# Kernel optimization log

Hardware: AMD Instinct MI355X
Metric: run time of the kernel (lower is better)

The kernel has to match this reference:

```python
import jax, jax.numpy as jnp
import numpy as np
import math

B, T, D = 2, 2048, 1024
H = 16
d = D // H
I = 2816
RMS_EPS = 1e-6
GN_EPS = 1e-5


def setup_inputs() -> dict:
    key = jax.random.key(0)
    ks = jax.random.split(key, 12)
    s = 0.02
    gammas = 1.0 - jnp.exp(jnp.linspace(math.log(0.1), math.log(0.001), H)).astype(jnp.float32)
    return {
        "x": jax.random.normal(ks[0], (B, T, D), dtype=jnp.float32),
        "ln1_w": jnp.ones((D,), jnp.float32),
        "ln2_w": jnp.ones((D,), jnp.float32),
        "Wq": jax.random.normal(ks[1], (D, D), jnp.float32) * s,
        "Wk": jax.random.normal(ks[2], (D, D), jnp.float32) * s,
        "Wv": jax.random.normal(ks[3], (D, D), jnp.float32) * s,
        "Wg": jax.random.normal(ks[4], (D, D), jnp.float32) * s,
        "Wo": jax.random.normal(ks[5], (D, D), jnp.float32) * s,
        "gamma": gammas,
        "gn_w": jnp.ones((D,), jnp.float32),
        "gn_b": jnp.zeros((D,), jnp.float32),
        "gate_w": jax.random.normal(ks[6], (I, D), jnp.float32) * s,
        "up_w": jax.random.normal(ks[7], (I, D), jnp.float32) * s,
        "down_w": jax.random.normal(ks[8], (D, I), jnp.float32) * s,
    }


def _rmsnorm(x, w):
    var = jnp.mean(x * x, axis=-1, keepdims=True)
    return (x * jax.lax.rsqrt(var + RMS_EPS)) * w


def _retnet_scan(q, k, v, gamma):
    # q,k,v: (B,T,H,d); gamma: (H,)
    qT = jnp.moveaxis(q, 1, 0)  # (T,B,H,d)
    kT = jnp.moveaxis(k, 1, 0)
    vT = jnp.moveaxis(v, 1, 0)

    def step(S, qkv_t):
        q_t, k_t, v_t = qkv_t
        # S: (B,H,d,d) ; outer product k_t v_t^T
        S = gamma[None, :, None, None] * S + k_t[..., :, None] * v_t[..., None, :]
        o_t = jnp.einsum('bhd,bhde->bhe', q_t, S)
        return S, o_t

    S0 = jnp.zeros((q.shape[0], H, d, d), q.dtype)
    _, yT = jax.lax.scan(step, S0, (qT, kT, vT))  # yT: (T,B,H,d)
    return jnp.moveaxis(yT, 0, 1)  # (B,T,H,d)


def _group_norm(y, gn_w, gn_b):
    # y: (B,T,H,d). torch GroupNorm(H groups) on (B,D,T): normalize per (b, head)
    # over the (T, d) extent.
    mean = jnp.mean(y, axis=(1, 3), keepdims=True)
    var = jnp.var(y, axis=(1, 3), keepdims=True)
    yn = (y - mean) * jax.lax.rsqrt(var + GN_EPS)
    return yn * gn_w.reshape(1, 1, H, d) + gn_b.reshape(1, 1, H, d)


def reference(x, ln1_w, ln2_w, Wq, Wk, Wv, Wg, Wo, gamma, gn_w, gn_b, gate_w, up_w, down_w):
    Bx, Tx, Dx = x.shape
    h = _rmsnorm(x, ln1_w)
    q = (h @ Wq.T).reshape(Bx, Tx, H, d)
    k = (h @ Wk.T).reshape(Bx, Tx, H, d)
    v = (h @ Wv.T).reshape(Bx, Tx, H, d)
    g = jax.nn.sigmoid(h @ Wg.T)
    gam = jax.nn.sigmoid(gamma)
    y = _retnet_scan(q, k, v, gam)          # (B,T,H,d)
    y = _group_norm(y, gn_w, gn_b).reshape(Bx, Tx, Dx)
    y = g * y
    x = x + y @ Wo.T
    h2 = _rmsnorm(x, ln2_w)
    mlp = (jax.nn.silu(h2 @ gate_w.T) * (h2 @ up_w.T)) @ down_w.T
    return x + mlp
```

## Files before the change

### kernel.cpp

```cpp
#include <hip/hip_runtime.h>
#include <hip/hip_bf16.h>
#include <cstdint>
#include <cstddef>

typedef __bf16 bf16_t;
typedef __bf16 bf16x4 __attribute__((ext_vector_type(4)));
typedef __bf16 bf16x8 __attribute__((ext_vector_type(8)));
typedef float f32x4 __attribute__((ext_vector_type(4)));

#define DEVINL __device__ __forceinline__

#define TT 2048
#define DD 1024
#define HH 16
#define II 2816

DEVINL float waveSum(float v) {
#pragma unroll
  for (int m = 32; m >= 1; m >>= 1) v += __shfl_xor(v, m, 64);
  return v;
}

DEVINL float sigmoidf_(float z) { return 1.0f / (1.0f + __expf(-z)); }

DEVINL void gload_lds16(const bf16_t* g, bf16_t* l) {
  __builtin_amdgcn_global_load_lds((const __attribute__((address_space(1))) void*)g,
                                   (__attribute__((address_space(3))) void*)l, 16, 0, 0);
}

__global__ __launch_bounds__(256) void prep_kernel(const float* __restrict__ Wq,
                                                   const float* __restrict__ Wk,
                                                   const float* __restrict__ Wv,
                                                   const float* __restrict__ Wg,
                                                   const float* __restrict__ Wo,
                                                   const float* __restrict__ gate_w,
                                                   const float* __restrict__ up_w,
                                                   const float* __restrict__ down_w,
                                                   bf16_t* __restrict__ Wqkvg_bf,
                                                   bf16_t* __restrict__ Wo_bf,
                                                   bf16_t* __restrict__ GU_bf,
                                                   bf16_t* __restrict__ down_bf,
                                                   float* __restrict__ stats) {
  const int bid = blockIdx.x;
  const int tid = threadIdx.x;
  if (bid == 0 && tid < 64) stats[tid] = 0.f;
  if (bid < 5120) {
    const int which = bid >> 10;
    const float* src;
    bf16_t* dst;
    switch (which) {
      case 0: src = Wq; dst = Wqkvg_bf; break;
      case 1: src = Wk; dst = Wqkvg_bf + (size_t)DD * DD; break;
      case 2: src = Wv; dst = Wqkvg_bf + 2 * (size_t)DD * DD; break;
      case 3: src = Wg; dst = Wqkvg_bf + 3 * (size_t)DD * DD; break;
      default: src = Wo; dst = Wo_bf; break;
    }
    const int i = (bid & 1023) * 256 + tid;
    float4 v = reinterpret_cast<const float4*>(src)[i];
    bf16x4 o;
    o[0] = (bf16_t)v.x; o[1] = (bf16_t)v.y; o[2] = (bf16_t)v.z; o[3] = (bf16_t)v.w;
    reinterpret_cast<bf16x4*>(dst)[i] = o;
  } else if (bid < 10752) {
    const int r = bid - 5120;
    const int jb = r >> 5, s = r & 31;
    const float* src = (s < 16) ? (gate_w + (size_t)(jb * 16 + s) * DD)
                                : (up_w + (size_t)(jb * 16 + s - 16) * DD);
    float4 v = reinterpret_cast<const float4*>(src)[tid];
    bf16x4 o;
    o[0] = (bf16_t)v.x; o[1] = (bf16_t)v.y; o[2] = (bf16_t)v.z; o[3] = (bf16_t)v.w;
    reinterpret_cast<bf16x4*>(GU_bf + (size_t)r * DD)[tid] = o;
  } else {
    const int i = (bid - 10752) * 256 + tid;
    float4 v = reinterpret_cast<const float4*>(down_w)[i];
    bf16x4 o;
    o[0] = (bf16_t)v.x; o[1] = (bf16_t)v.y; o[2] = (bf16_t)v.z; o[3] = (bf16_t)v.w;
    reinterpret_cast<bf16x4*>(down_bf)[i] = o;
  }
}

__global__ __launch_bounds__(256) void rmsnorm_kernel(const float* __restrict__ x,
                                                      const float* __restrict__ w,
                                                      bf16_t* __restrict__ out) {
  const int row = blockIdx.x;
  const int tid = threadIdx.x;
  const float4 v = reinterpret_cast<const float4*>(x + (size_t)row * DD)[tid];
  float ss = v.x * v.x + v.y * v.y + v.z * v.z + v.w * v.w;
  ss = waveSum(ss);
  __shared__ float red[4];
  if ((tid & 63) == 0) red[tid >> 6] = ss;
  __syncthreads();
  const float total = red[0] + red[1] + red[2] + red[3];
  const float rstd = rsqrtf(total * (1.0f / (float)DD) + 1e-6f);
  const float4 wv = reinterpret_cast<const float4*>(w)[tid];
  bf16x4 o;
  o[0] = (bf16_t)(v.x * rstd * wv.x);
  o[1] = (bf16_t)(v.y * rstd * wv.y);
  o[2] = (bf16_t)(v.z * rstd * wv.z);
  o[3] = (bf16_t)(v.w * rstd * wv.w);
  reinterpret_cast<bf16x4*>(out + (size_t)row * DD)[tid] = o;
}

template <int EPI>
__global__ __launch_bounds__(512, 4) void gemm128x256(const bf16_t* __restrict__ A,
                                                      const bf16_t* __restrict__ B,
                                                      bf16_t* __restrict__ O1,
                                                      bf16_t* __restrict__ O2,
                                                      int M, int N, int K) {
  extern __shared__ __align__(16) char lds[];
  const int tid = threadIdx.x;
  const int wid = tid >> 6;
  const int lane = tid & 63;
  const int wr = wid >> 2;
  const int wc = wid & 3;

  const int gx = gridDim.x;
  const int nwg = gx * gridDim.y;
  int flat = blockIdx.y * gx + blockIdx.x;
  flat = (flat & 7) * (nwg >> 3) + (flat >> 3);
  const int row0 = (flat / gx) * 128;
  const int col0 = (flat % gx) * 256;

  const int ls_row = lane >> 2;
  const int ls_col = ((lane & 3) ^ ((lane >> 3) & 3)) * 8;
  const bf16_t* gA = A + (size_t)(row0 + wid * 16 + ls_row) * K + ls_col;
  const bf16_t* gB = B + (size_t)(col0 + wid * 32 + ls_row) * K + ls_col;

  const int kq = lane >> 4;
  const int rl = lane & 15;
  const int xg = (rl >> 1) & 3;
  const int gsel = (kq ^ xg) << 4;

  f32x4 acc[4][4] = {};
  const int nt = K >> 5;

  auto stage = [&](int t) {
    char* slot = lds + (t % 3) * 24576;
    const int ko = t << 5;
    gload_lds16(gA + ko, (bf16_t*)(slot + wid * 1024));
#pragma unroll
    for (int j = 0; j < 2; ++j)
      gload_lds16(gB + (size_t)j * 16 * K + ko,
                  (bf16_t*)(slot + 8192 + wid * 2048 + j * 1024));
  };

  stage(0); stage(1);
  asm volatile("s_waitcnt vmcnt(3)" ::: "memory");
  __builtin_amdgcn_s_barrier();
  __builtin_amdgcn_sched_barrier(0);

  for (int t = 0; t < nt; ++t) {
    if (t + 2 < nt) stage(t + 2);
    const char* ab = lds + (t % 3) * 24576;
    const char* bb = ab + 8192;
    bf16x8 aF[4], bF[4];
#pragma unroll
    for (int n = 0; n < 4; ++n)
      bF[n] = *reinterpret_cast<const bf16x8*>(bb + (wc * 64 + n * 16 + rl) * 64 + gsel);
#pragma unroll
    for (int m = 0; m < 4; ++m)
      aF[m] = *reinterpret_cast<const bf16x8*>(ab + (wr * 64 + m * 16 + rl) * 64 + gsel);
    __builtin_amdgcn_s_setprio(1);
#pragma unroll
    for (int m = 0; m < 4; ++m)
#pragma unroll
      for (int n = 0; n < 4; ++n)
        acc[m][n] = __builtin_amdgcn_mfma_f32_16x16x32_bf16(aF[m], bF[n], acc[m][n], 0, 0, 0);
    __builtin_amdgcn_s_setprio(0);
    if (t + 2 < nt) {
      asm volatile("s_waitcnt vmcnt(3)" ::: "memory");
    } else if (t + 2 == nt) {
      asm volatile("s_waitcnt vmcnt(0)" ::: "memory");
    }
    __builtin_amdgcn_s_barrier();
    __builtin_amdgcn_sched_barrier(0);
  }

  const int crow = row0 + wr * 64 + kq * 4;
  const int ccol = col0 + wc * 64 + rl;
  if (EPI == 2) {
    const int obase = (col0 + wc * 64) / 2 + rl;
#pragma unroll
    for (int m = 0; m < 4; ++m)
#pragma unroll
      for (int p = 0; p < 2; ++p)
#pragma unroll
        for (int r = 0; r < 4; ++r) {
          const float g = acc[m][2 * p][r];
          const float u = acc[m][2 * p + 1][r];
          O1[(size_t)(crow + m * 16 + r) * II + (obase + p * 16)] =
              (bf16_t)(g * sigmoidf_(g) * u);
        }
  } else {
    if (col0 < 3072) {
#pragma unroll
      for (int m = 0; m < 4; ++m)
#pragma unroll
        for (int n = 0; n < 4; ++n)
#pragma unroll
          for (int r = 0; r < 4; ++r)
            O1[(size_t)(crow + m * 16 + r) * 3072 + (ccol + n * 16)] = (bf16_t)acc[m][n][r];
    } else {
#pragma unroll
      for (int m = 0; m < 4; ++m)
#pragma unroll
        for (int n = 0; n < 4; ++n)
#pragma unroll
          for (int r = 0; r < 4; ++r)
            O2[(size_t)(crow + m * 16 + r) * DD + (ccol + n * 16 - 3072)] =
                (bf16_t)sigmoidf_(acc[m][n][r]);
    }
  }
}

__global__ __launch_bounds__(256) void gemm64x128(const bf16_t* __restrict__ A,
                                                  const bf16_t* __restrict__ B,
                                                  float* __restrict__ C,
                                                  const float* __restrict__ addsrc,
                                                  int M, int N, int K) {
  __shared__ __align__(16) bf16_t smA[64 * 32];
  __shared__ __align__(16) bf16_t smB[128 * 32];
  const int tid = threadIdx.x;
  const int wid = tid >> 6;
  const int lane = tid & 63;
  const int row0 = blockIdx.y * 64;
  const int col0 = blockIdx.x * 128;

  f32x4 acc[4][2] = {};

  const int ls_row = lane >> 2;
  const int ls_col = ((lane & 3) ^ ((lane >> 3) & 3)) * 8;
  const bf16_t* gA = A + (size_t)(row0 + wid * 16 + ls_row) * K + ls_col;
  const bf16_t* gB = B + (size_t)(col0 + wid * 32 + ls_row) * K + ls_col;

  const int rl = lane & 15;
  const int kq = lane >> 4;
  const int xg = (rl >> 1) & 3;
  const int ge = (kq ^ xg) * 8;

  for (int k0 = 0; k0 < K; k0 += 32) {
    gload_lds16(gA + k0, smA + wid * 512);
#pragma unroll
    for (int j = 0; j < 2; ++j)
      gload_lds16(gB + (size_t)j * 16 * K + k0, smB + wid * 1024 + j * 512);
    __syncthreads();
    bf16x8 aF[4], bF[2];
#pragma unroll
    for (int m = 0; m < 4; ++m)
      aF[m] = *reinterpret_cast<const bf16x8*>(smA + (m * 16 + rl) * 32 + ge);
#pragma unroll
    for (int n = 0; n < 2; ++n)
      bF[n] = *reinterpret_cast<const bf16x8*>(smB + (wid * 32 + n * 16 + rl) * 32 + ge);
#pragma unroll
    for (int m = 0; m < 4; ++m)
#pragma unroll
      for (int n = 0; n < 2; ++n)
        acc[m][n] = __builtin_amdgcn_mfma_f32_16x16x32_bf16(aF[m], bF[n], acc[m][n], 0, 0, 0);
    __syncthreads();
  }

  const int ccol = col0 + wid * 32 + rl;
#pragma unroll
  for (int m = 0; m < 4; ++m)
#pragma unroll
    for (int n = 0; n < 2; ++n)
#pragma unroll
      for (int r = 0; r < 4; ++r) {
        const size_t idx = (size_t)(row0 + m * 16 + kq * 4 + r) * N + (ccol + n * 16);
        C[idx] = acc[m][n][r] + addsrc[idx];
      }
}

__global__ __launch_bounds__(256) void retscan_mfma(const bf16_t* __restrict__ qkv,
                                                    const float* __restrict__ gamma,
                                                    float* __restrict__ y,
                                                    float* __restrict__ stats) {
  const int c = blockIdx.x;
  const int bh = blockIdx.y;
  const int b = bh >> 4;
  const int h = bh & 15;
  const int tid = threadIdx.x;
  const int w = tid >> 6;
  const int lane = tid & 63;
  const int kq = lane >> 4;
  const int rl = lane & 15;

  __shared__ __align__(16) bf16_t K_lds[128 * 64];
  __shared__ __align__(16) bf16_t VT_lds[64 * 128];
  __shared__ __align__(16) bf16_t P_lds[64 * 128];
  __shared__ float rs[4][2];

  const size_t rstr = 3 * DD;
  const bf16_t* base = qkv + (size_t)(b * TT) * rstr + h * 64;
  const bf16_t* kgl = base + DD;
  const bf16_t* vgl = base + 2 * DD;

  for (int g = tid; g < 1024; g += 256) {
    const int sw = g >> 3, gr = g & 7;
    const int t = c * 64 - 64 + sw;
    bf16x8 kv = {};
    bf16x8 vv = {};
    if (t >= 0) {
      kv = *reinterpret_cast<const bf16x8*>(kgl + (size_t)t * rstr + gr * 8);
      vv = *reinterpret_cast<const bf16x8*>(vgl + (size_t)t * rstr + gr * 8);
    }
    *reinterpret_cast<bf16x8*>(K_lds + sw * 64 + ((gr ^ (sw & 7)) << 3)) = kv;
#pragma unroll
    for (int j = 0; j < 8; ++j) {
      const int e = gr * 8 + j;
      const int gs = (sw >> 3) ^ (e & 7);
      VT_lds[e * 128 + (gs << 3) + (sw & 7)] = vv[j];
    }
  }

  const int i0 = w * 16;
  const bf16_t* qrow = base + (size_t)(c * 64 + i0 + rl) * rstr;
  bf16x8 qF0 = *reinterpret_cast<const bf16x8*>(qrow + kq * 8);
  bf16x8 qF1 = *reinterpret_cast<const bf16x8*>(qrow + 32 + kq * 8);
  const float gam = sigmoidf_(gamma[h]);
  const float l2g = __log2f(gam);
  const float gi16 = exp2f(-16.f * l2g);

  __syncthreads();

  f32x4 S[8];
#pragma unroll
  for (int st = 0; st < 8; ++st) {
    const int sw = st * 16 + rl;
    const bf16_t* krow = K_lds + sw * 64;
    bf16x8 kF0 = *reinterpret_cast<const bf16x8*>(krow + ((kq ^ (sw & 7)) << 3));
    bf16x8 kF1 = *reinterpret_cast<const bf16x8*>(krow + (((4 + kq) ^ (sw & 7)) << 3));
    f32x4 s = {};
    s = __builtin_amdgcn_mfma_f32_16x16x32_bf16(qF0, kF0, s, 0, 0, 0);
    s = __builtin_amdgcn_mfma_f32_16x16x32_bf16(qF1, kF1, s, 0, 0, 0);
    S[st] = s;
  }

  float wgt[4];
  int lag[4];
#pragma unroll
  for (int r = 0; r < 4; ++r) {
    lag[r] = 64 + i0 + kq * 4 + r - rl;
    wgt[r] = exp2f((float)lag[r] * l2g);
  }
#pragma unroll
  for (int st = 0; st < 8; ++st) {
    const int sw = st * 16 + rl;
#pragma unroll
    for (int r = 0; r < 4; ++r) {
      const float p = (lag[r] >= 0) ? S[st][r] * wgt[r] : 0.f;
      const int i = i0 + kq * 4 + r;
      const int gs = (sw >> 3) ^ (i & 7);
      P_lds[i * 128 + (gs << 3) + (sw & 7)] = (bf16_t)p;
      lag[r] -= 16;
      wgt[r] *= gi16;
    }
  }
  asm volatile("s_waitcnt lgkmcnt(0)" ::: "memory");
  __builtin_amdgcn_sched_barrier(0);

  f32x4 Y[4] = {};
#pragma unroll
  for (int ks = 0; ks < 4; ++ks) {
    const int ia = i0 + rl;
    const int ga = (ks * 4 + kq) ^ (ia & 7);
    bf16x8 aF = *reinterpret_cast<const bf16x8*>(P_lds + ia * 128 + (ga << 3));
#pragma unroll
    for (int et = 0; et < 4; ++et) {
      const int e = et * 16 + rl;
      const int gb = (ks * 4 + kq) ^ (e & 7);
      bf16x8 bF = *reinterpret_cast<const bf16x8*>(VT_lds + e * 128 + (gb << 3));
      Y[et] = __builtin_amdgcn_mfma_f32_16x16x32_bf16(aF, bF, Y[et], 0, 0, 0);
    }
  }

  float s = 0.f, ss = 0.f;
  const size_t ybase = (size_t)(b * TT + c * 64 + i0 + kq * 4) * DD + h * 64 + rl;
#pragma unroll
  for (int et = 0; et < 4; ++et)
#pragma unroll
    for (int r = 0; r < 4; ++r) {
      const float v = Y[et][r];
      s += v;
      ss += v * v;
      y[ybase + (size_t)r * DD + et * 16] = v;
    }
  s = waveSum(s);
  ss = waveSum(ss);
  if (lane == 0) { rs[w][0] = s; rs[w][1] = ss; }
  __syncthreads();
  if (tid == 0) {
    atomicAdd(&stats[bh * 2], rs[0][0] + rs[1][0] + rs[2][0] + rs[3][0]);
    atomicAdd(&stats[bh * 2 + 1], rs[0][1] + rs[1][1] + rs[2][1] + rs[3][1]);
  }
}

__global__ __launch_bounds__(256) void gn_apply_kernel(const float* __restrict__ y,
                                                       const float* __restrict__ stats,
                                                       const bf16_t* __restrict__ gsig,
                                                       const float* __restrict__ gn_w,
                                                       const float* __restrict__ gn_b,
                                                       bf16_t* __restrict__ out) {
  const int row = blockIdx.x;
  const int tid = threadIdx.x;
  const int col = tid * 4;
  const int b = row >> 11;
  const int h = col >> 6;
  const float S = stats[(b * HH + h) * 2];
  const float SS = stats[(b * HH + h) * 2 + 1];
  const float inv = 1.0f / ((float)TT * 64.0f);
  const float mean = S * inv;
  const float var = SS * inv - mean * mean;
  const float rstd = rsqrtf(var + 1e-5f);
  float4 v = reinterpret_cast<const float4*>(y + (size_t)row * DD)[tid];
  float4 wv = reinterpret_cast<const float4*>(gn_w)[tid];
  float4 bv = reinterpret_cast<const float4*>(gn_b)[tid];
  bf16x4 gv = reinterpret_cast<const bf16x4*>(gsig + (size_t)row * DD)[tid];
  bf16x4 o;
  o[0] = (bf16_t)((((v.x - mean) * rstd) * wv.x + bv.x) * (float)gv[0]);
  o[1] = (bf16_t)((((v.y - mean) * rstd) * wv.y + bv.y) * (float)gv[1]);
  o[2] = (bf16_t)((((v.z - mean) * rstd) * wv.z + bv.z) * (float)gv[2]);
  o[3] = (bf16_t)((((v.w - mean) * rstd) * wv.w + bv.w) * (float)gv[3]);
  reinterpret_cast<bf16x4*>(out + (size_t)row * DD)[tid] = o;
}

extern "C" void kernel_launch(void* const* d_in, const int* in_sizes, int n_in,
                              void* d_out, int out_size, void* d_ws, size_t ws_size,
                              hipStream_t stream) {
  const float* x = (const float*)d_in[0];
  const float* ln1_w = (const float*)d_in[1];
  const float* ln2_w = (const float*)d_in[2];
  const float* Wq = (const float*)d_in[3];
  const float* Wk = (const float*)d_in[4];
  const float* Wv = (const float*)d_in[5];
  const float* Wg = (const float*)d_in[6];
  const float* Wo = (const float*)d_in[7];
  const float* gamma = (const float*)d_in[8];
  const float* gn_w = (const float*)d_in[9];
  const float* gn_b = (const float*)d_in[10];
  const float* gate_w = (const float*)d_in[11];
  const float* up_w = (const float*)d_in[12];
  const float* down_w = (const float*)d_in[13];
  float* out = (float*)d_out;

  const int M = 2 * TT;

  char* ws = (char*)d_ws;
  size_t off = 0;
  auto alloc = [&](size_t bytes) -> void* {
    void* p = ws + off;
    off += (bytes + 255) & ~(size_t)255;
    return p;
  };
  bf16_t* h_bf = (bf16_t*)alloc((size_t)M * DD * 2);
  bf16_t* Wqkvg_bf = (bf16_t*)alloc((size_t)4 * DD * DD * 2);
  bf16_t* Wo_bf = (bf16_t*)alloc((size_t)DD * DD * 2);
  bf16_t* GU_bf = (bf16_t*)alloc((size_t)2 * II * DD * 2);
  bf16_t* down_bf = (bf16_t*)alloc((size_t)DD * II * 2);
  bf16_t* qkv_bf = (bf16_t*)alloc((size_t)M * 3 * DD * 2);
  bf16_t* gsig = (bf16_t*)alloc((size_t)M * DD * 2);
  float* yBuf = (float*)alloc((size_t)M * DD * 4);
  bf16_t* ygated = (bf16_t*)alloc((size_t)M * DD * 2);
  bf16_t* act = (bf16_t*)alloc((size_t)M * II * 2);
  float* stats = (float*)alloc(64 * 4);
  (void)ws_size; (void)in_sizes; (void)n_in; (void)out_size;

  float* x2 = yBuf;

  prep_kernel<<<13568, 256, 0, stream>>>(Wq, Wk, Wv, Wg, Wo, gate_w, up_w, down_w,
                                         Wqkvg_bf, Wo_bf, GU_bf, down_bf, stats);

  rmsnorm_kernel<<<M, 256, 0, stream>>>(x, ln1_w, h_bf);

  {
    dim3 g(4 * DD / 256, M / 128);
    gemm128x256<3><<<g, 512, 73728, stream>>>(h_bf, Wqkvg_bf, qkv_bf, gsig, M, 4 * DD, DD);
  }

  {
    dim3 g(TT / 64, 2 * HH);
    retscan_mfma<<<g, 256, 0, stream>>>(qkv_bf, gamma, yBuf, stats);
  }

  gn_apply_kernel<<<M, 256, 0, stream>>>(yBuf, stats, gsig, gn_w, gn_b, ygated);

  {
    dim3 g(DD / 128, M / 64);
    gemm64x128<<<g, 256, 0, stream>>>(ygated, Wo_bf, x2, x, M, DD, DD);
  }

  rmsnorm_kernel<<<M, 256, 0, stream>>>(x2, ln2_w, h_bf);

  {
    dim3 g(2 * II / 256, M / 128);
    gemm128x256<2><<<g, 512, 73728, stream>>>(h_bf, GU_bf, act, nullptr, M, 2 * II, DD);
  }

  {
    dim3 g(DD / 128, M / 64);
    gemm64x128<<<g, 256, 0, stream>>>(act, down_bf, out, x2, M, DD, II);
  }
}
```

Before: 246.9 us.

## Pipeline gemm64x128 with 5-slot LDS ring and swizzled block order

Replaces the single-buffer load/sync loop in gemm64x128 with a 5-stage LDS ring buffer that keeps four K-tiles of global-to-LDS loads in flight. It uses explicit vmcnt waits and one barrier per iteration in place of two __syncthreads. It also remaps block indices so consecutive blocks walk down rows sharing a column of B, and raises wave priority around the MFMA burst. This aims to hide global memory latency in this GEMM, at the cost of more LDS (60 KB), which may reduce occupancy. Correctness relies on the hardcoded grid shape (8 in x, 64 row tiles).

```diff
diff --git a/kernel.cpp b/kernel.cpp
--- a/kernel.cpp
+++ b/kernel.cpp
@@ -217,13 +217,13 @@
                                                   float* __restrict__ C,
                                                   const float* __restrict__ addsrc,
                                                   int M, int N, int K) {
-  __shared__ __align__(16) bf16_t smA[64 * 32];
-  __shared__ __align__(16) bf16_t smB[128 * 32];
+  __shared__ __align__(16) bf16_t sm[5 * 6144];
   const int tid = threadIdx.x;
   const int wid = tid >> 6;
   const int lane = tid & 63;
-  const int row0 = blockIdx.y * 64;
-  const int col0 = blockIdx.x * 128;
+  const int d = blockIdx.y * 8 + blockIdx.x;
+  const int row0 = (d & 63) * 64;
+  const int col0 = (d >> 6) * 128;
 
   f32x4 acc[4][2] = {};
 
@@ -237,25 +237,49 @@
   const int xg = (rl >> 1) & 3;
   const int ge = (kq ^ xg) * 8;
 
-  for (int k0 = 0; k0 < K; k0 += 32) {
-    gload_lds16(gA + k0, smA + wid * 512);
+  const int nt = K >> 5;
+  auto stage = [&](int t) {
+    bf16_t* slot = sm + (t % 5) * 6144;
+    const int ko = t << 5;
+    gload_lds16(gA + ko, slot + wid * 512);
 #pragma unroll
     for (int j = 0; j < 2; ++j)
-      gload_lds16(gB + (size_t)j * 16 * K + k0, smB + wid * 1024 + j * 512);
-    __syncthreads();
+      gload_lds16(gB + (size_t)j * 16 * K + ko, slot + 2048 + wid * 1024 + j * 512);
+  };
+
+  stage(0); stage(1); stage(2); stage(3);
+  asm volatile("s_waitcnt vmcnt(9)" ::: "memory");
+  __builtin_amdgcn_s_barrier();
+  __builtin_amdgcn_sched_barrier(0);
+
+  for (int t = 0; t < nt; ++t) {
+    if (t + 5 <= nt) stage(t + 4);
+    const bf16_t* slot = sm + (t % 5) * 6144;
     bf16x8 aF[4], bF[2];
 #pragma unroll
     for (int m = 0; m < 4; ++m)
-      aF[m] = *reinterpret_cast<const bf16x8*>(smA + (m * 16 + rl) * 32 + ge);
+      aF[m] = *reinterpret_cast<const bf16x8*>(slot + (m * 16 + rl) * 32 + ge);
 #pragma unroll
     for (int n = 0; n < 2; ++n)
-      bF[n] = *reinterpret_cast<const bf16x8*>(smB + (wid * 32 + n * 16 + rl) * 32 + ge);
+      bF[n] = *reinterpret_cast<const bf16x8*>(slot + 2048 + (wid * 32 + n * 16 + rl) * 32 + ge);
+    __builtin_amdgcn_s_setprio(1);
 #pragma unroll
     for (int m = 0; m < 4; ++m)
 #pragma unroll
       for (int n = 0; n < 2; ++n)
         acc[m][n] = __builtin_amdgcn_mfma_f32_16x16x32_bf16(aF[m], bF[n], acc[m][n], 0, 0, 0);
-    __syncthreads();
+    __builtin_amdgcn_s_setprio(0);
+    if (t + 5 <= nt) {
+      asm volatile("s_waitcnt vmcnt(9)" ::: "memory");
+    } else if (t + 4 == nt) {
+      asm volatile("s_waitcnt vmcnt(6)" ::: "memory");
+    } else if (t + 3 == nt) {
+      asm volatile("s_waitcnt vmcnt(3)" ::: "memory");
+    } else if (t + 2 == nt) {
+      asm volatile("s_waitcnt vmcnt(0)" ::: "memory");
+    }
+    __builtin_amdgcn_s_barrier();
+    __builtin_amdgcn_sched_barrier(0);
   }
 
   const int ccol = col0 + wid * 32 + rl;
```

New measurement: 222.8 us. 9.8% less time.
